# Kernel optimization log

Hardware: AMD Instinct MI355X
Metric: run time of the kernel (lower is better)

## Reference

```python
import jax, jax.numpy as jnp
import numpy as np


def setup_inputs() -> dict:
    key = jax.random.key(0)
    ks = jax.random.split(key, 9)
    B, T, S, E, H = 4, 4096, 4096, 512, 64
    return {
        "x": jax.random.normal(ks[0], (B, T, 1), dtype=jnp.float32),
        "tok_emb": jax.random.normal(ks[1], (B, S, E), dtype=jnp.float32),
        "key_w": jax.random.normal(ks[2], (H, E), dtype=jnp.float32) * 0.05,
        "key_b": jax.random.normal(ks[3], (H,), dtype=jnp.float32) * 0.05,
        "query_w": jax.random.normal(ks[4], (H, 1), dtype=jnp.float32) * 0.05,
        "query_b": jax.random.normal(ks[5], (H,), dtype=jnp.float32) * 0.05,
        "value_w": jax.random.normal(ks[6], (H, E), dtype=jnp.float32) * 0.05,
        "proj_w": jax.random.normal(ks[7], (1, H), dtype=jnp.float32) * 0.05,
        "proj_b": jax.random.normal(ks[8], (1,), dtype=jnp.float32) * 0.05,
    }


def reference(x, tok_emb, key_w, key_b, query_w, query_b, value_w, proj_w, proj_b):
    # k = tanh(Linear(tok_emb))            [B,S,H]
    k = jnp.tanh(jnp.einsum("bse,he->bsh", tok_emb, key_w) + key_b)
    # q = tanh(Linear(x)); x last dim is 1 [B,T,H]
    q = jnp.tanh(jnp.einsum("btu,hu->bth", x, query_w) + query_b)
    scale = k.shape[-1] ** (-0.5)
    wei = jnp.einsum("bth,bsh->bts", q, k) * scale  # [B,T,S]
    # NOTE: softmax over dim=-2 (the query/T axis), faithful to the original
    wei = jax.nn.softmax(wei, axis=-2)
    v = jnp.tanh(jnp.einsum("bse,he->bsh", tok_emb, value_w))  # [B,S,H]
    out = jnp.tanh(jnp.einsum("bts,bsh->bth", wei, v))         # [B,T,H]
    out = jnp.einsum("bth,oh->bto", out, proj_w) + proj_b      # [B,T,1]
    return jnp.squeeze(out, axis=-1)                            # [B,T]
```

## Files before the change

kernel.cpp:

```cpp
#include <hip/hip_runtime.h>
#include <math.h>

#define BB 4
#define TT 4096
#define SS 4096
#define EE 512
#define HH 64
#define NN 128
#define XR 6.0f


typedef __attribute__((ext_vector_type(8))) __bf16 bf16x8;
typedef __attribute__((ext_vector_type(16))) float f32x16;

__device__ __forceinline__ unsigned short f2b(float f) {
  unsigned int u = __float_as_uint(f);
  return (unsigned short)((u + 0x7FFFu + ((u >> 16) & 1u)) >> 16);
}

__device__ __forceinline__ float fast_tanh(float v) {
  float e = __expf(fminf(60.0f, 2.0f * v));
  return (e - 1.0f) * __builtin_amdgcn_rcpf(e + 1.0f);
}

__global__ __launch_bounds__(256) void prep_sm_kernel(
    const float* __restrict__ kw, const float* __restrict__ vw,
    const float* __restrict__ qw, const float* __restrict__ qb,
    const float* __restrict__ x, unsigned int* __restrict__ Wfrag,
    float* __restrict__ Cmat, unsigned short* __restrict__ qnA,
    float* __restrict__ Sm_part, float* __restrict__ Oz) {
  const int blk = blockIdx.x;
  if (blk < 64) {
    int idx = blk * 256 + threadIdx.x;
    int jq = idx & 1;
    int l = (idx >> 1) & 63;
    int ks = (idx >> 7) & 31;
    int nb = idx >> 12;
    int n = nb * 32 + (l & 31);
    int k = ks * 16 + (l >> 5) * 8 + jq * 4;
    const float* row = (n < HH) ? (kw + n * EE + k) : (vw + (n - HH) * EE + k);
    float4 wv = *(const float4*)row;
    Wfrag[idx * 2] = (unsigned int)f2b(wv.x) | ((unsigned int)f2b(wv.y) << 16);
    Wfrag[idx * 2 + 1] =
        (unsigned int)f2b(wv.z) | ((unsigned int)f2b(wv.w) << 16);
  } else if (blk < 128) {
    int idx = (blk - 64) * 256 + threadIdx.x;
    int m = idx >> 7;
    int j = idx & (NN - 1);
    int k = (m * (2 * j + 1)) & 511;
    if (k >= 256) k -= 512;
    Cmat[idx] = cosf((float)k * (float)(M_PI / 256.0));
    if (idx < 8192) ((float4*)Oz)[idx] = make_float4(0.f, 0.f, 0.f, 0.f);
    if (idx < 8192) {
      int h = idx & 63;
      int j2 = idx >> 6;
      float th = (float)M_PI * ((float)j2 + 0.5f) * (1.0f / NN);
      float xj = XR * cosf(th);
      float val = tanhf(fmaf(xj, qw[h], qb[h]));
      int pos =
          (((j2 >> 5) * 4 + (h >> 4)) * 64 + (j2 & 31) + 32 * ((h >> 3) & 1)) *
              8 +
          (h & 7);
      qnA[pos] = f2b(val);
    }
  } else {
    __shared__ float Tm[128][NN + 1];
    int blk2 = blk - 128;
    int b = blk2 >> 5;
    int chunk = blk2 & 31;
    int tid = threadIdx.x;
    if (tid < 128) {
      float xh = x[b * TT + chunk * 128 + tid] * (1.0f / XR);
      xh = fminf(1.0f, fmaxf(-1.0f, xh));
      Tm[tid][0] = 1.0f;
      Tm[tid][1] = xh;
      float x2 = 2.0f * xh;
      float tm2 = 1.0f, tm1 = xh;
#pragma unroll 6
      for (int m = 2; m < NN; ++m) {
        float t = fmaf(x2, tm1, -tm2);
        Tm[tid][m] = t;
        tm2 = tm1;
        tm1 = t;
      }
    }
    __syncthreads();
    if (tid < 128) {
      float s = 0.f;
#pragma unroll 8
      for (int i = 0; i < 128; ++i) s += Tm[i][tid];
      Sm_part[(b * 32 + chunk) * NN + tid] = s;
    }
  }
}

__global__ __launch_bounds__(256) void kvattn_kernel(
    const float* __restrict__ emb, const float* __restrict__ kb,
    const unsigned int* __restrict__ Wfrag, const unsigned short* __restrict__ qnA,
    const float* __restrict__ Cmat, const float* __restrict__ Sm_part,
    float* __restrict__ O) {
  __shared__ __align__(16) char smem[69120];
  unsigned short* A_lds = (unsigned short*)smem;
  unsigned short* ktB = (unsigned short*)smem;
  unsigned short* vB = (unsigned short*)(smem + 8192);
  unsigned short* eA = (unsigned short*)(smem + 16384);
  float* zred = (float*)(smem + 65536);
  float* wql = (float*)(smem + 67840);
  float* izl = (float*)(smem + 68352);
  float* sml = (float*)(smem + 68608);

  const int tid = threadIdx.x;
  const int row0 = blockIdx.x * 64;
  const int bb = row0 >> 12;

#pragma unroll
  for (int mb = 0; mb < 2; ++mb) {
    int m = tid >> 3;
    int c8 = tid & 7;
    const float* src = emb + (size_t)(row0 + mb * 32 + m) * EE;
    unsigned short* dst = A_lds + mb * 16384;
    float4 buf[16];
#pragma unroll
    for (int it = 0; it < 16; ++it) buf[it] = *(const float4*)(src + (c8 + it * 8) * 4);
#pragma unroll
    for (int it = 0; it < 16; ++it) {
      int k = (c8 + it * 8) * 4;
      float4 v = buf[it];
      int kstep = k >> 4;
      int lane = m + 32 * ((k >> 3) & 1);
      int j = k & 7;
      unsigned int lo = (unsigned int)f2b(v.x) | ((unsigned int)f2b(v.y) << 16);
      unsigned int hi = (unsigned int)f2b(v.z) | ((unsigned int)f2b(v.w) << 16);
      *(uint2*)&dst[(kstep * 64 + lane) * 8 + j] = make_uint2(lo, hi);
    }
  }
  if (tid < 128) {
    float s = 0.f;
#pragma unroll 8
    for (int c = 0; c < 32; ++c) s += Sm_part[(bb * 32 + c) * NN + tid];
    sml[tid] = s * ((tid == 0) ? (1.0f / NN) : (2.0f / NN));
  }
  __syncthreads();
  if (tid < 128) {
    float a0 = 0.f, a1 = 0.f, a2 = 0.f, a3 = 0.f;
#pragma unroll
    for (int m = 0; m < NN; m += 4) {
      a0 = fmaf(sml[m], Cmat[m * NN + tid], a0);
      a1 = fmaf(sml[m + 1], Cmat[(m + 1) * NN + tid], a1);
      a2 = fmaf(sml[m + 2], Cmat[(m + 2) * NN + tid], a2);
      a3 = fmaf(sml[m + 3], Cmat[(m + 3) * NN + tid], a3);
    }
    wql[tid] = (a0 + a1) + (a2 + a3);
  }

  const int w = tid >> 6;
  const int lane = tid & 63;
  f32x16 acc0 = {}, acc1 = {};
  const bf16x8* Bf = (const bf16x8*)Wfrag;
#pragma unroll 4
  for (int kstep = 0; kstep < 32; ++kstep) {
    bf16x8 bfr = Bf[(w * 32 + kstep) * 64 + lane];
    bf16x8 a0 = *(const bf16x8*)&A_lds[(kstep * 64 + lane) * 8];
    bf16x8 a1 = *(const bf16x8*)&A_lds[16384 + (kstep * 64 + lane) * 8];
    acc0 = __builtin_amdgcn_mfma_f32_32x32x16_bf16(a0, bfr, acc0, 0, 0, 0);
    acc1 = __builtin_amdgcn_mfma_f32_32x32x16_bf16(a1, bfr, acc1, 0, 0, 0);
  }
  __syncthreads();

  {
    const int n = w * 32 + (lane & 31);
    if (w < 2) {
      float kbv = kb[n];
      const int ks_h = n >> 4;
      const int off_h = 32 * ((n >> 3) & 1);
      const int jj_h = n & 7;
#pragma unroll
      for (int reg = 0; reg < 16; ++reg) {
        int sl = (reg & 3) + 8 * (reg >> 2) + 4 * (lane >> 5);
        ktB[(ks_h * 64 + sl + off_h) * 8 + jj_h] =
            f2b(fast_tanh(acc0[reg] + kbv));
        ktB[((4 + ks_h) * 64 + sl + off_h) * 8 + jj_h] =
            f2b(fast_tanh(acc1[reg] + kbv));
      }
    } else {
      int h = n - 64;
      const int nb_h = h >> 5;
      const int lm = h & 31;
#pragma unroll
      for (int reg = 0; reg < 16; ++reg) {
        int sl = (reg & 3) + 8 * (reg >> 2) + 4 * (lane >> 5);
        int s1 = sl + 32;
        vB[((nb_h * 4 + (sl >> 4)) * 64 + lm + 32 * ((sl >> 3) & 1)) * 8 +
           (sl & 7)] = f2b(fast_tanh(acc0[reg]));
        vB[((nb_h * 4 + (s1 >> 4)) * 64 + lm + 32 * ((s1 >> 3) & 1)) * 8 +
           (s1 & 7)] = f2b(fast_tanh(acc1[reg]));
      }
    }
  }
  __syncthreads();

  f32x16 l0 = {}, l1 = {};
#pragma unroll
  for (int ks = 0; ks < 4; ++ks) {
    bf16x8 a = *(const bf16x8*)(qnA + ((w * 4 + ks) * 64 + lane) * 8);
    bf16x8 b0 = *(const bf16x8*)&ktB[(ks * 64 + lane) * 8];
    bf16x8 b1 = *(const bf16x8*)&ktB[((4 + ks) * 64 + lane) * 8];
    l0 = __builtin_amdgcn_mfma_f32_32x32x16_bf16(a, b0, l0, 0, 0, 0);
    l1 = __builtin_amdgcn_mfma_f32_32x32x16_bf16(a, b1, l1, 0, 0, 0);
  }
  float e0[16], e1[16];
  float zp0 = 0.f, zp1 = 0.f;
#pragma unroll
  for (int r = 0; r < 4; ++r) {
    float4 wq4 = *(const float4*)&wql[w * 32 + 8 * r + 4 * (lane >> 5)];
    float wa[4] = {wq4.x, wq4.y, wq4.z, wq4.w};
#pragma unroll
    for (int c = 0; c < 4; ++c) {
      int reg = 4 * r + c;
      e0[reg] = __expf(l0[reg] * 0.125f);
      e1[reg] = __expf(l1[reg] * 0.125f);
      zp0 = fmaf(wa[c], e0[reg], zp0);
      zp1 = fmaf(wa[c], e1[reg], zp1);
    }
  }
  zred[(lane & 31) * 9 + w * 2 + (lane >> 5)] = zp0;
  zred[(32 + (lane & 31)) * 9 + w * 2 + (lane >> 5)] = zp1;
  __syncthreads();
  if (tid < 64) {
    float sum = 0.f;
#pragma unroll
    for (int k = 0; k < 8; ++k) sum += zred[tid * 9 + k];
    izl[tid] = 1.0f / sum;
  }
  __syncthreads();

  {
    const int sA = lane & 31, sB = 32 + (lane & 31);
    const float izA = izl[sA], izB = izl[sB];
    const int ksA = sA >> 4, oA = 32 * ((sA >> 3) & 1), jA = sA & 7;
    const int ksB = sB >> 4, oB = 32 * ((sB >> 3) & 1), jB = sB & 7;
#pragma unroll
    for (int reg = 0; reg < 16; ++reg) {
      int jl = (reg & 3) + 8 * (reg >> 2) + 4 * (lane >> 5);
      eA[((w * 4 + ksA) * 64 + jl + oA) * 8 + jA] = f2b(e0[reg] * izA);
      eA[((w * 4 + ksB) * 64 + jl + oB) * 8 + jB] = f2b(e1[reg] * izB);
    }
  }
  __syncthreads();
  f32x16 o0 = {}, o1 = {};
#pragma unroll
  for (int ks = 0; ks < 4; ++ks) {
    bf16x8 a = *(const bf16x8*)&eA[((w * 4 + ks) * 64 + lane) * 8];
    bf16x8 b0 = *(const bf16x8*)&vB[(ks * 64 + lane) * 8];
    bf16x8 b1 = *(const bf16x8*)&vB[((4 + ks) * 64 + lane) * 8];
    o0 = __builtin_amdgcn_mfma_f32_32x32x16_bf16(a, b0, o0, 0, 0, 0);
    o1 = __builtin_amdgcn_mfma_f32_32x32x16_bf16(a, b1, o1, 0, 0, 0);
  }
  float* op = O + (size_t)bb * (NN * HH);
  const int h0 = lane & 31, h1 = 32 + (lane & 31);
#pragma unroll
  for (int reg = 0; reg < 16; ++reg) {
    int j = w * 32 + (reg & 3) + 8 * (reg >> 2) + 4 * (lane >> 5);
    atomicAdd(&op[j * HH + h0], o0[reg]);
    atomicAdd(&op[j * HH + h1], o1[reg]);
  }
}

__global__ __launch_bounds__(256) void final_kernel(
    const float* __restrict__ x, const float* __restrict__ O,
    const float* __restrict__ pw, const float* __restrict__ pb,
    const float* __restrict__ Cmat, float* __restrict__ y) {
  const int idx = blockIdx.x * 256 + threadIdx.x;
  const int b = idx >> 12;
  __shared__ float yl[NN];
  __shared__ float c[NN];
  {
    const int j = threadIdx.x >> 1;
    const int half = threadIdx.x & 1;
    const float4* Ov =
        (const float4*)(O + ((size_t)(b * NN + j) * HH + half * 32));
    const float4* pwv = (const float4*)(pw + half * 32);
    float s = 0.f;
#pragma unroll
    for (int q = 0; q < 8; ++q) {
      float4 ov = Ov[q];
      float4 pv = pwv[q];
      s += fast_tanh(ov.x) * pv.x + fast_tanh(ov.y) * pv.y +
           fast_tanh(ov.z) * pv.z + fast_tanh(ov.w) * pv.w;
    }
    s += __shfl_xor(s, 1, 64);
    if (half == 0) yl[j] = s + pb[0];
  }
  __syncthreads();
  if (threadIdx.x < NN) {
    int m = threadIdx.x;
    double acc = 0.0;
#pragma unroll 8
    for (int j = 0; j < NN; ++j)
      acc += (double)yl[j] * (double)Cmat[m * NN + j];
    c[m] = (float)(acc * ((m == 0 ? 1.0 : 2.0) / NN));
  }
  __syncthreads();
  float xf = x[idx] * (1.0f / XR);
  xf = fminf(1.0f, fmaxf(-1.0f, xf));
  double xh = (double)xf;
  double b1 = 0.0, b2 = 0.0;
  for (int m = NN - 1; m >= 1; --m) {
    double t = fma(2.0 * xh, b1, (double)c[m] - b2);
    b2 = b1;
    b1 = t;
  }
  y[idx] = (float)fma(xh, b1, (double)c[0] - b2);
}

extern "C" void kernel_launch(void* const* d_in, const int* in_sizes, int n_in,
                              void* d_out, int out_size, void* d_ws,
                              size_t ws_size, hipStream_t stream) {
  const float* x = (const float*)d_in[0];
  const float* emb = (const float*)d_in[1];
  const float* kw = (const float*)d_in[2];
  const float* kb = (const float*)d_in[3];
  const float* qw = (const float*)d_in[4];
  const float* qb = (const float*)d_in[5];
  const float* vw = (const float*)d_in[6];
  const float* pw = (const float*)d_in[7];
  const float* pb = (const float*)d_in[8];

  float* ws = (float*)d_ws;
  float* O = ws;
  float* Cmat = ws + 32768;
  unsigned short* qnA = (unsigned short*)(Cmat + 16384);
  unsigned int* Wfrag = (unsigned int*)(Cmat + 16384 + 4096);
  float* Sm_part = (float*)(Wfrag + 32768);
  float* y = (float*)d_out;

  prep_sm_kernel<<<256, 256, 0, stream>>>(kw, vw, qw, qb, x, Wfrag, Cmat, qnA,
                                          Sm_part, O);
  kvattn_kernel<<<BB * SS / 64, 256, 0, stream>>>(emb, kb, Wfrag, qnA, Cmat,
                                                  Sm_part, O);
  final_kernel<<<BB * TT / 256, 256, 0, stream>>>(x, O, pw, pb, Cmat, y);
}
```

Measured before the change: 117.7 us.

## Split kvattn row halves across eight waves with 512-thread blocks

Doubles the kvattn block from 256 to 512 threads. Each wave now handles one 32-row half of the 64-row tile instead of both halves, so the embedding load, the K/V projection MFMA loop, the score MFMAs and the output MFMAs are spread over 8 waves. With a grid of only 256 blocks, and likely about one block per CU, the aim is more in-flight waves per CU to hide global-load and MFMA latency, plus fewer accumulator registers per thread. The cost is less instruction-level parallelism per wave, since the two interleaved MFMA chains become one, and more waves contend at each barrier.

```diff
diff --git a/kernel.cpp b/kernel.cpp
--- a/kernel.cpp
+++ b/kernel.cpp
@@ -94,7 +94,7 @@
   }
 }
 
-__global__ __launch_bounds__(256) void kvattn_kernel(
+__global__ __launch_bounds__(512) void kvattn_kernel(
     const float* __restrict__ emb, const float* __restrict__ kb,
     const unsigned int* __restrict__ Wfrag, const unsigned short* __restrict__ qnA,
     const float* __restrict__ Cmat, const float* __restrict__ Sm_part,
@@ -113,25 +113,26 @@
   const int row0 = blockIdx.x * 64;
   const int bb = row0 >> 12;
 
-#pragma unroll
-  for (int mb = 0; mb < 2; ++mb) {
+  {
     int m = tid >> 3;
     int c8 = tid & 7;
-    const float* src = emb + (size_t)(row0 + mb * 32 + m) * EE;
-    unsigned short* dst = A_lds + mb * 16384;
+    const float* src = emb + (size_t)(row0 + m) * EE;
+    unsigned short* dst = A_lds + (m >> 5) * 16384;
+    int ml = m & 31;
     float4 buf[16];
 #pragma unroll
-    for (int it = 0; it < 16; ++it) buf[it] = *(const float4*)(src + (c8 + it * 8) * 4);
+    for (int it = 0; it < 16; ++it)
+      buf[it] = *(const float4*)(src + (c8 + it * 8) * 4);
 #pragma unroll
     for (int it = 0; it < 16; ++it) {
       int k = (c8 + it * 8) * 4;
       float4 v = buf[it];
       int kstep = k >> 4;
-      int lane = m + 32 * ((k >> 3) & 1);
+      int lane_f = ml + 32 * ((k >> 3) & 1);
       int j = k & 7;
       unsigned int lo = (unsigned int)f2b(v.x) | ((unsigned int)f2b(v.y) << 16);
       unsigned int hi = (unsigned int)f2b(v.z) | ((unsigned int)f2b(v.w) << 16);
-      *(uint2*)&dst[(kstep * 64 + lane) * 8 + j] = make_uint2(lo, hi);
+      *(uint2*)&dst[(kstep * 64 + lane_f) * 8 + j] = make_uint2(lo, hi);
     }
   }
   if (tid < 128) {
@@ -153,17 +154,18 @@
     wql[tid] = (a0 + a1) + (a2 + a3);
   }
 
-  const int w = tid >> 6;
+  const int w8 = tid >> 6;
   const int lane = tid & 63;
-  f32x16 acc0 = {}, acc1 = {};
+  const int w = w8 & 3;
+  const int mh = w8 >> 2;
+  f32x16 acc = {};
   const bf16x8* Bf = (const bf16x8*)Wfrag;
+  const unsigned short* Ah = A_lds + mh * 16384;
 #pragma unroll 4
   for (int kstep = 0; kstep < 32; ++kstep) {
     bf16x8 bfr = Bf[(w * 32 + kstep) * 64 + lane];
-    bf16x8 a0 = *(const bf16x8*)&A_lds[(kstep * 64 + lane) * 8];
-    bf16x8 a1 = *(const bf16x8*)&A_lds[16384 + (kstep * 64 + lane) * 8];
-    acc0 = __builtin_amdgcn_mfma_f32_32x32x16_bf16(a0, bfr, acc0, 0, 0, 0);
-    acc1 = __builtin_amdgcn_mfma_f32_32x32x16_bf16(a1, bfr, acc1, 0, 0, 0);
+    bf16x8 a = *(const bf16x8*)&Ah[(kstep * 64 + lane) * 8];
+    acc = __builtin_amdgcn_mfma_f32_32x32x16_bf16(a, bfr, acc, 0, 0, 0);
   }
   __syncthreads();
 
@@ -177,10 +179,8 @@
 #pragma unroll
       for (int reg = 0; reg < 16; ++reg) {
         int sl = (reg & 3) + 8 * (reg >> 2) + 4 * (lane >> 5);
-        ktB[(ks_h * 64 + sl + off_h) * 8 + jj_h] =
-            f2b(fast_tanh(acc0[reg] + kbv));
-        ktB[((4 + ks_h) * 64 + sl + off_h) * 8 + jj_h] =
-            f2b(fast_tanh(acc1[reg] + kbv));
+        ktB[((mh * 4 + ks_h) * 64 + sl + off_h) * 8 + jj_h] =
+            f2b(fast_tanh(acc[reg] + kbv));
       }
     } else {
       int h = n - 64;
@@ -189,27 +189,23 @@
 #pragma unroll
       for (int reg = 0; reg < 16; ++reg) {
         int sl = (reg & 3) + 8 * (reg >> 2) + 4 * (lane >> 5);
-        int s1 = sl + 32;
-        vB[((nb_h * 4 + (sl >> 4)) * 64 + lm + 32 * ((sl >> 3) & 1)) * 8 +
-           (sl & 7)] = f2b(fast_tanh(acc0[reg]));
-        vB[((nb_h * 4 + (s1 >> 4)) * 64 + lm + 32 * ((s1 >> 3) & 1)) * 8 +
-           (s1 & 7)] = f2b(fast_tanh(acc1[reg]));
+        int s = mh * 32 + sl;
+        vB[((nb_h * 4 + (s >> 4)) * 64 + lm + 32 * ((s >> 3) & 1)) * 8 +
+           (s & 7)] = f2b(fast_tanh(acc[reg]));
       }
     }
   }
   __syncthreads();
 
-  f32x16 l0 = {}, l1 = {};
+  f32x16 l0 = {};
 #pragma unroll
   for (int ks = 0; ks < 4; ++ks) {
     bf16x8 a = *(const bf16x8*)(qnA + ((w * 4 + ks) * 64 + lane) * 8);
-    bf16x8 b0 = *(const bf16x8*)&ktB[(ks * 64 + lane) * 8];
-    bf16x8 b1 = *(const bf16x8*)&ktB[((4 + ks) * 64 + lane) * 8];
+    bf16x8 b0 = *(const bf16x8*)&ktB[((mh * 4 + ks) * 64 + lane) * 8];
     l0 = __builtin_amdgcn_mfma_f32_32x32x16_bf16(a, b0, l0, 0, 0, 0);
-    l1 = __builtin_amdgcn_mfma_f32_32x32x16_bf16(a, b1, l1, 0, 0, 0);
-  }
-  float e0[16], e1[16];
-  float zp0 = 0.f, zp1 = 0.f;
+  }
+  float e0[16];
+  float zp = 0.f;
 #pragma unroll
   for (int r = 0; r < 4; ++r) {
     float4 wq4 = *(const float4*)&wql[w * 32 + 8 * r + 4 * (lane >> 5)];
@@ -218,13 +214,10 @@
     for (int c = 0; c < 4; ++c) {
       int reg = 4 * r + c;
       e0[reg] = __expf(l0[reg] * 0.125f);
-      e1[reg] = __expf(l1[reg] * 0.125f);
-      zp0 = fmaf(wa[c], e0[reg], zp0);
-      zp1 = fmaf(wa[c], e1[reg], zp1);
-    }
-  }
-  zred[(lane & 31) * 9 + w * 2 + (lane >> 5)] = zp0;
-  zred[(32 + (lane & 31)) * 9 + w * 2 + (lane >> 5)] = zp1;
+      zp = fmaf(wa[c], e0[reg], zp);
+    }
+  }
+  zred[(mh * 32 + (lane & 31)) * 9 + w * 2 + (lane >> 5)] = zp;
   __syncthreads();
   if (tid < 64) {
     float sum = 0.f;
@@ -235,34 +228,31 @@
   __syncthreads();
 
   {
-    const int sA = lane & 31, sB = 32 + (lane & 31);
-    const float izA = izl[sA], izB = izl[sB];
-    const int ksA = sA >> 4, oA = 32 * ((sA >> 3) & 1), jA = sA & 7;
-    const int ksB = sB >> 4, oB = 32 * ((sB >> 3) & 1), jB = sB & 7;
+    const int s = mh * 32 + (lane & 31);
+    const float iz = izl[s];
+    const int q0 = w * 4 + (s >> 4);
+    const int lof = 32 * ((s >> 3) & 1);
+    const int idx = s & 7;
 #pragma unroll
     for (int reg = 0; reg < 16; ++reg) {
       int jl = (reg & 3) + 8 * (reg >> 2) + 4 * (lane >> 5);
-      eA[((w * 4 + ksA) * 64 + jl + oA) * 8 + jA] = f2b(e0[reg] * izA);
-      eA[((w * 4 + ksB) * 64 + jl + oB) * 8 + jB] = f2b(e1[reg] * izB);
-    }
-  }
-  __syncthreads();
-  f32x16 o0 = {}, o1 = {};
+      eA[(q0 * 64 + jl + lof) * 8 + idx] = f2b(e0[reg] * iz);
+    }
+  }
+  __syncthreads();
+  f32x16 o0 = {};
 #pragma unroll
   for (int ks = 0; ks < 4; ++ks) {
     bf16x8 a = *(const bf16x8*)&eA[((w * 4 + ks) * 64 + lane) * 8];
-    bf16x8 b0 = *(const bf16x8*)&vB[(ks * 64 + lane) * 8];
-    bf16x8 b1 = *(const bf16x8*)&vB[((4 + ks) * 64 + lane) * 8];
+    bf16x8 b0 = *(const bf16x8*)&vB[((mh * 4 + ks) * 64 + lane) * 8];
     o0 = __builtin_amdgcn_mfma_f32_32x32x16_bf16(a, b0, o0, 0, 0, 0);
-    o1 = __builtin_amdgcn_mfma_f32_32x32x16_bf16(a, b1, o1, 0, 0, 0);
   }
   float* op = O + (size_t)bb * (NN * HH);
-  const int h0 = lane & 31, h1 = 32 + (lane & 31);
+  const int h0 = mh * 32 + (lane & 31);
 #pragma unroll
   for (int reg = 0; reg < 16; ++reg) {
     int j = w * 32 + (reg & 3) + 8 * (reg >> 2) + 4 * (lane >> 5);
     atomicAdd(&op[j * HH + h0], o0[reg]);
-    atomicAdd(&op[j * HH + h1], o1[reg]);
   }
 }
 
@@ -336,7 +326,7 @@
 
   prep_sm_kernel<<<256, 256, 0, stream>>>(kw, vw, qw, qb, x, Wfrag, Cmat, qnA,
                                           Sm_part, O);
-  kvattn_kernel<<<BB * SS / 64, 256, 0, stream>>>(emb, kb, Wfrag, qnA, Cmat,
+  kvattn_kernel<<<BB * SS / 64, 512, 0, stream>>>(emb, kb, Wfrag, qnA, Cmat,
                                                   Sm_part, O);
   final_kernel<<<BB * TT / 256, 256, 0, stream>>>(x, O, pw, pb, Cmat, y);
 }
```

Result: no change. 116.1 us (-1.4%).
